# Optimization experiments

Measured on AMD Instinct MI355X. Metric: run time of the kernel, lower is better.

## Reference

```python
import jax, jax.numpy as jnp
import numpy as np

WH = WW = 7          # window size
N_TOK = WH * WW      # 49 tokens per window
HEADS = 8
HEAD_DIM = 32
DIM = HEADS * HEAD_DIM  # 256
NW = 64              # windows per image (56x56 / 7x7)
BW = 64 * NW         # batch_images * windows = 4096


def _rel_pos_index(wh, ww):
    # Swin-style relative position index, flattened to (N*N,)
    coords = np.stack(np.meshgrid(np.arange(wh), np.arange(ww), indexing='ij'))  # (2, wh, ww)
    coords = coords.reshape(2, -1)                                               # (2, N)
    rel = coords[:, :, None] - coords[:, None, :]                                # (2, N, N)
    rel = rel.transpose(1, 2, 0).astype(np.int64)                                # (N, N, 2)
    rel[:, :, 0] += wh - 1
    rel[:, :, 1] += ww - 1
    rel[:, :, 0] *= 2 * ww - 1
    return jnp.asarray(rel.sum(-1).reshape(-1))                                  # (N*N,)

_REL_IDX = _rel_pos_index(WH, WW)


def setup_inputs() -> dict:
    key = jax.random.key(0)
    ks = jax.random.split(key, 5)
    x = jax.random.normal(ks[0], (BW, N_TOK, DIM), dtype=jnp.float32)
    mask = jnp.zeros((1, NW, 1, N_TOK, N_TOK), dtype=jnp.float32)
    w_qkv = jax.random.normal(ks[1], (DIM, 3 * HEADS * HEAD_DIM), dtype=jnp.float32) * 0.02
    b_qkv = jnp.zeros((3 * HEADS * HEAD_DIM,), dtype=jnp.float32)
    rel_table = jax.random.normal(ks[2], ((2 * WH - 1) * (2 * WW - 1), HEADS), dtype=jnp.float32) * 0.02
    w_out = jax.random.normal(ks[3], (HEADS * HEAD_DIM, DIM), dtype=jnp.float32) * 0.02
    b_out = jnp.zeros((DIM,), dtype=jnp.float32)
    return {"x": x, "mask": mask, "w_qkv": w_qkv, "b_qkv": b_qkv,
            "rel_table": rel_table, "w_out": w_out, "b_out": b_out}


def reference(x, mask, w_qkv, b_qkv, rel_table, w_out, b_out):
    bw, n, d = x.shape
    # QKV projection then split per original Rearrange:
    # 'b n (qkv h hd) -> qkv b h n hd'
    qkv = (x @ w_qkv + b_qkv).reshape(bw, n, 3, HEADS, HEAD_DIM)
    qkv = qkv.transpose(2, 0, 3, 1, 4)  # (3, bw, h, n, hd)
    q, k, v = qkv[0], qkv[1], qkv[2]
    # NOTE: original computes einsum('bnid,bnjd->bnij', k, q): a[i,j] = k_i . q_j
    a = jnp.einsum('bhid,bhjd->bhij', k, q) / jnp.sqrt(jnp.asarray(HEAD_DIM, x.dtype))
    # relative position bias: table gather then '(i j) h -> h i j'
    bias = rel_table[_REL_IDX].reshape(n, n, HEADS).transpose(2, 0, 1)  # (h, n, n)
    a = a + bias
    # mask add: '(b nW) h i j -> b nW h i j', + mask, back
    nw = mask.shape[1]
    a = a.reshape(bw // nw, nw, HEADS, n, n) + mask
    a = a.reshape(bw, HEADS, n, n)
    a = jax.nn.softmax(a, axis=-1)
    y = jnp.einsum('bhij,bhjd->bhid', a, v)        # (bw, h, n, hd)
    y = y.transpose(0, 2, 1, 3).reshape(bw, n, HEADS * HEAD_DIM)
    return y @ w_out + b_out
```

## Files before the change

kernel.cpp:

```cpp
#include <hip/hip_runtime.h>

typedef __attribute__((ext_vector_type(8))) short short8;
typedef __attribute__((ext_vector_type(4))) float f32x4;
typedef unsigned short u16;

#define NTOK 49
#define NBLK 4096
#define LOG2E 1.4426950408889634f

#define XF  0
#define QKP 16384
#define VTF 49152
#define POOLN 65536

#define WS_WQT 0
#define WS_WOT 393216
#define WS_BQS 524288
#define WS_BIAS 528384
#define WS_MKG 659456
#define WS_CMB 1708032
#define WS_NEED (WS_CMB + 8388608)

__device__ __forceinline__ u16 f2bf(float f) {
  unsigned u = __float_as_uint(f);
  return (u16)((u + 0x7fffu + ((u >> 16) & 1u)) >> 16);
}
__device__ __forceinline__ unsigned packbf(float a, float b) {
  unsigned r;
  asm("v_cvt_pk_bf16_f32 %0, %1, %2" : "=v"(r) : "v"(a), "v"(b));
  return r;
}

__global__ void prep_kernel(const float* __restrict__ w_qkv,
                            const float* __restrict__ w_out,
                            const float* __restrict__ rel,
                            const float* __restrict__ mask,
                            const float* __restrict__ b_qkv,
                            u16* __restrict__ wqTf,
                            u16* __restrict__ woTf,
                            float* __restrict__ bqs,
                            float* __restrict__ biasf,
                            float* __restrict__ mkg) {
  const float SCQ = 0.17677669529663687f * LOG2E;
  const int stride = gridDim.x * blockDim.x;
  const int gid = blockIdx.x * blockDim.x + threadIdx.x;
  for (int e = gid; e < 48 * 8 * 64 * 8; e += stride) {
    int eL = e & 7, ln = (e >> 3) & 63, ks = (e >> 9) & 7, ctg = e >> 12;
    int k = ks * 32 + (ln >> 4) * 8 + eL;
    int c = ctg * 16 + (ln & 15);
    float wv = w_qkv[k * 768 + c];
    if (ctg < 16) wv *= SCQ;
    wqTf[e] = f2bf(wv);
  }
  for (int e = gid; e < 16 * 8 * 64 * 8; e += stride) {
    int eL = e & 7, ln = (e >> 3) & 63, ks = (e >> 9) & 7, ctg = e >> 12;
    int k = ks * 32 + (ln >> 4) * 8 + eL;
    int c = ctg * 16 + (ln & 15);
    woTf[e] = f2bf(w_out[k * 256 + c]);
  }
  for (int e = gid; e < 768; e += stride)
    bqs[e] = b_qkv[e] * (e < 256 ? SCQ : 1.f);
  for (int e = gid; e < 8 * 16 * 64 * 4; e += stride) {
    int rg = e & 3, ln = (e >> 2) & 63, t = (e >> 8) & 15, hh = e >> 12;
    int i = (t >> 2) * 16 + (ln & 15);
    int j = (t & 3) * 16 + (ln >> 4) * 4 + rg;
    float v;
    if (j >= NTOK) v = -1e30f;
    else if (i >= NTOK) v = 0.f;
    else {
      int dh = i / 7 - j / 7 + 6;
      int dw = i % 7 - j % 7 + 6;
      v = rel[(dh * 13 + dw) * 8 + hh];
    }
    biasf[e] = v * LOG2E;
  }
  for (int e = gid; e < 64 * 16 * 64 * 4; e += stride) {
    int rg = e & 3, ln = (e >> 2) & 63, t = (e >> 8) & 15, wdw = e >> 12;
    int i = (t >> 2) * 16 + (ln & 15);
    int j = (t & 3) * 16 + (ln >> 4) * 4 + rg;
    mkg[e] = (i < NTOK && j < NTOK) ? mask[wdw * (NTOK * NTOK) + i * NTOK + j] * LOG2E : 0.f;
  }
}

__global__ void prep2_kernel(const float* __restrict__ biasf,
                             const float* __restrict__ mkg,
                             float* __restrict__ cmb) {
  const int stride = gridDim.x * blockDim.x;
  for (int e = blockIdx.x * blockDim.x + threadIdx.x; e < 64 * 8 * 4096; e += stride) {
    int x = e & 4095, hh = (e >> 12) & 7, wdw = e >> 15;
    cmb[e] = biasf[hh * 4096 + x] + mkg[wdw * 4096 + x];
  }
}

__global__ void __launch_bounds__(1024, 4) winattn_mfma(
    const float* __restrict__ x,
    const float* __restrict__ bqs,
    const float* __restrict__ b_out,
    const u16* __restrict__ wqTf,
    const u16* __restrict__ woTf,
    const float* __restrict__ biasf,
    const float* __restrict__ mkg,
    const float* __restrict__ cmb,
    float* __restrict__ out)
{
  __shared__ u16 pool[POOLN];
  const int b = blockIdx.x, tid = threadIdx.x;
  const int lane = tid & 63, lo = lane & 15, hi = lane >> 4;
  const int w = tid >> 6;
  const int h = w & 7;
  const int it0 = (w >> 3) * 2;
  const f32x4 zf = {0.f, 0.f, 0.f, 0.f};

  {
    const float4* xg = (const float4*)(x + (size_t)b * (NTOK * 256));
    for (int e = tid; e < 49 * 64; e += 1024) {
      float4 v = xg[e];
      int r = e >> 6, c4 = (e & 63) << 2;
      int addr = (((r >> 4) * 8 + (c4 >> 5)) * 64 + ((c4 >> 3) & 3) * 16 + (r & 15)) * 8 + (c4 & 7);
      *(uint2*)&pool[XF + addr] = make_uint2(packbf(v.x, v.y), packbf(v.z, v.w));
    }
    if (tid < 15 * 64) {
      int e = tid;
      int r = 49 + (e >> 6), c4 = (e & 63) << 2;
      int addr = (((r >> 4) * 8 + (c4 >> 5)) * 64 + ((c4 >> 3) & 3) * 16 + (r & 15)) * 8 + (c4 & 7);
      *(uint2*)&pool[XF + addr] = make_uint2(0u, 0u);
    }
  }
  __syncthreads();

  {
    const int ctq0 = 2 * w, ctq1 = 2 * w + 1, ctv = 32 + w;
    f32x4 acc[3][4];
    #pragma unroll
    for (int ct = 0; ct < 3; ++ct)
      #pragma unroll
      for (int rt = 0; rt < 4; ++rt) acc[ct][rt] = zf;
    #pragma unroll
    for (int ks = 0; ks < 8; ++ks) {
      short8 bx[4];
      #pragma unroll
      for (int rt = 0; rt < 4; ++rt)
        bx[rt] = *(const short8*)&pool[XF + ((rt * 8 + ks) * 64 + lane) * 8];
      short8 af0 = *(const short8*)&wqTf[((size_t)(ctq0 * 8 + ks) * 64 + lane) * 8];
      short8 af1 = *(const short8*)&wqTf[((size_t)(ctq1 * 8 + ks) * 64 + lane) * 8];
      short8 afv = *(const short8*)&wqTf[((size_t)(ctv * 8 + ks) * 64 + lane) * 8];
      #pragma unroll
      for (int rt = 0; rt < 4; ++rt) {
        acc[0][rt] = __builtin_amdgcn_mfma_f32_16x16x32_bf16(af0, bx[rt], acc[0][rt], 0, 0, 0);
        acc[1][rt] = __builtin_amdgcn_mfma_f32_16x16x32_bf16(af1, bx[rt], acc[1][rt], 0, 0, 0);
        acc[2][rt] = __builtin_amdgcn_mfma_f32_16x16x32_bf16(bx[rt], afv, acc[2][rt], 0, 0, 0);
      }
    }
    const int qkbase = QKP + (w & 7) * 4096 + ((w >= 8) ? 2048 : 0);
    #pragma unroll
    for (int ct = 0; ct < 2; ++ct) {
      const int ctg = 2 * w + ct;
      f32x4 bias = *(const f32x4*)(bqs + ctg * 16 + hi * 4);
      #pragma unroll
      for (int rt = 0; rt < 4; ++rt) {
        f32x4 v = acc[ct][rt] + bias;
        int hi2 = ct * 2 + (hi >> 1);
        int eb = (hi & 1) * 4;
        *(uint2*)&pool[qkbase + (rt * 64 + hi2 * 16 + lo) * 8 + eb] =
            make_uint2(packbf(v[0], v[1]), packbf(v[2], v[3]));
      }
    }
    {
      const int vhead = w >> 1, dblk = w & 1;
      const float bv = bqs[ctv * 16 + lo];
      #pragma unroll
      for (int rt = 0; rt < 4; ++rt) {
        f32x4 v = acc[2][rt];
        float v0 = v[0] + bv, v1 = v[1] + bv, v2 = v[2] + bv, v3 = v[3] + bv;
        int f = dblk * 2 + (rt >> 1);
        int hiR = (rt & 1) * 2 + (hi >> 1);
        int eb = (hi & 1) * 4;
        *(uint2*)&pool[VTF + (f * 8 + vhead) * 512 + (hiR * 16 + lo) * 8 + eb] =
            make_uint2(packbf(v0, v1), packbf(v2, v3));
      }
    }
  }
  __syncthreads();

  short8 va[2][2];
  #pragma unroll
  for (int dblk = 0; dblk < 2; ++dblk)
    #pragma unroll
    for (int k2 = 0; k2 < 2; ++k2)
      va[dblk][k2] = *(const short8*)&pool[VTF + ((dblk * 2 + k2) * 8 + h) * 512 + lane * 8];
  __syncthreads();

  {
    short8 qa[4], ka[2];
    #pragma unroll
    for (int jt = 0; jt < 4; ++jt)
      qa[jt] = *(const short8*)&pool[QKP + h * 4096 + (jt * 64 + lane) * 8];
    #pragma unroll
    for (int itL = 0; itL < 2; ++itL)
      ka[itL] = *(const short8*)&pool[QKP + h * 4096 + 2048 + ((it0 + itL) * 64 + lane) * 8];
    const float* cb;
    const float* mb = nullptr;
    if (cmb) {
      cb = cmb + (((size_t)(b & 63) * 8 + h) << 12);
    } else {
      cb = biasf + h * 4096;
      mb = mkg + (size_t)(b & 63) * 4096;
    }
    #pragma unroll
    for (int itL = 0; itL < 2; ++itL) {
      float rs = 0.f;
      #pragma unroll
      for (int jt = 0; jt < 4; ++jt) {
        f32x4 s = __builtin_amdgcn_mfma_f32_16x16x32_bf16(qa[jt], ka[itL], zf, 0, 0, 0);
        const int t = (it0 + itL) * 4 + jt;
        f32x4 c4 = *(const f32x4*)&cb[(t * 64 + lane) * 4];
        if (mb) {
          f32x4 m4 = *(const f32x4*)&mb[(t * 64 + lane) * 4];
          c4[0] += m4[0]; c4[1] += m4[1]; c4[2] += m4[2]; c4[3] += m4[3];
        }
        float p0 = exp2f(s[0] + c4[0]);
        float p1 = exp2f(s[1] + c4[1]);
        float p2 = exp2f(s[2] + c4[2]);
        float p3 = exp2f(s[3] + c4[3]);
        rs += (p0 + p1) + (p2 + p3);
        int k2 = jt >> 1;
        int hi2 = (jt & 1) * 2 + (hi >> 1);
        int eb = (hi & 1) * 4;
        *(uint2*)&pool[VTF + ((it0 + k2) * 8 + h) * 512 + (hi2 * 16 + lo) * 8 + eb] =
            make_uint2(packbf(p0, p1), packbf(p2, p3));
      }
      float r2 = rs + __shfl_xor(rs, 16);
      const float inv = 1.f / (r2 + __shfl_xor(r2, 32));
      f32x4 ya0 = zf, ya1 = zf;
      #pragma unroll
      for (int k2 = 0; k2 < 2; ++k2) {
        short8 pb = *(const short8*)&pool[VTF + ((it0 + k2) * 8 + h) * 512 + lane * 8];
        ya0 = __builtin_amdgcn_mfma_f32_16x16x32_bf16(va[0][k2], pb, ya0, 0, 0, 0);
        ya1 = __builtin_amdgcn_mfma_f32_16x16x32_bf16(va[1][k2], pb, ya1, 0, 0, 0);
      }
      #pragma unroll
      for (int dblk = 0; dblk < 2; ++dblk) {
        f32x4 yy = dblk ? ya1 : ya0;
        int hi2 = dblk * 2 + (hi >> 1);
        int eb = (hi & 1) * 4;
        *(uint2*)&pool[XF + (((it0 + itL) * 8 + h) * 64 + hi2 * 16 + lo) * 8 + eb] =
            make_uint2(packbf(yy[0] * inv, yy[1] * inv), packbf(yy[2] * inv, yy[3] * inv));
      }
    }
  }
  __syncthreads();

  {
    f32x4 pacc[4];
    pacc[0] = zf; pacc[1] = zf; pacc[2] = zf; pacc[3] = zf;
    #pragma unroll
    for (int ks = 0; ks < 8; ++ks) {
      short8 wf = *(const short8*)&woTf[((size_t)(w * 8 + ks) * 64 + lane) * 8];
      #pragma unroll
      for (int rt = 0; rt < 4; ++rt) {
        short8 yb = *(const short8*)&pool[XF + ((rt * 8 + ks) * 64 + lane) * 8];
        pacc[rt] = __builtin_amdgcn_mfma_f32_16x16x32_bf16(wf, yb, pacc[rt], 0, 0, 0);
      }
    }
    float* og = out + (size_t)b * (NTOK * 256);
    const int cb2 = w * 16 + hi * 4;
    f32x4 bb = *(const f32x4*)(b_out + cb2);
    #pragma unroll
    for (int rt = 0; rt < 4; ++rt) {
      const int r = rt * 16 + lo;
      if (r < NTOK) {
        f32x4 vv = pacc[rt] + bb;
        *(f32x4*)(og + (size_t)r * 256 + cb2) = vv;
      }
    }
  }
}

extern "C" void kernel_launch(void* const* d_in, const int* in_sizes, int n_in,
                              void* d_out, int out_size, void* d_ws, size_t ws_size,
                              hipStream_t stream) {
  const float *x = nullptr, *mask = nullptr, *w_qkv = nullptr, *b_qkv = nullptr,
              *rel_t = nullptr, *w_out = nullptr, *b_out = nullptr;
  for (int i = 0; i < n_in; ++i) {
    const float* p = (const float*)d_in[i];
    switch (in_sizes[i]) {
      case 4096 * 49 * 256: x = p; break;
      case 64 * 49 * 49:    mask = p; break;
      case 256 * 768:       w_qkv = p; break;
      case 768:             b_qkv = p; break;
      case 169 * 8:         rel_t = p; break;
      case 256 * 256:       w_out = p; break;
      case 256:             b_out = p; break;
    }
  }
  char* wsb = (char*)d_ws;
  u16* wqTf    = (u16*)(wsb + WS_WQT);
  u16* woTf    = (u16*)(wsb + WS_WOT);
  float* bqs   = (float*)(wsb + WS_BQS);
  float* biasf = (float*)(wsb + WS_BIAS);
  float* mkg   = (float*)(wsb + WS_MKG);
  const bool fits = (ws_size >= (size_t)WS_NEED);
  float* cmb   = fits ? (float*)(wsb + WS_CMB) : nullptr;

  hipLaunchKernelGGL(prep_kernel, dim3(1024), dim3(256), 0, stream,
                     w_qkv, w_out, rel_t, mask, b_qkv, wqTf, woTf, bqs, biasf, mkg);
  if (fits) {
    hipLaunchKernelGGL(prep2_kernel, dim3(2048), dim3(256), 0, stream,
                       biasf, mkg, cmb);
  }
  hipLaunchKernelGGL(winattn_mfma, dim3(NBLK), dim3(1024), 0, stream,
                     x, bqs, b_out, wqTf, woTf, biasf, mkg, cmb, (float*)d_out);
}
```

Measured before the change: 279.1 us.

## Process two windows per block and prefetch second window's input during attention

Each 1024-thread block now handles two consecutive windows instead of one, halving the grid. The second window's x tile is loaded and converted to bf16 into a free region of shared memory while the first window's softmax and PV stage runs, so global load latency can overlap with compute. The shared-memory layout is remapped so the second window's QK buffers avoid the staged x region. The cost is extra barriers and fewer blocks in flight, which gives the scheduler less parallelism to hide latency across the GPU.

```diff
diff --git a/kernel.cpp b/kernel.cpp
--- a/kernel.cpp
+++ b/kernel.cpp
@@ -5,11 +5,8 @@
 typedef unsigned short u16;
 
 #define NTOK 49
-#define NBLK 4096
 #define LOG2E 1.4426950408889634f
 
-#define XF  0
-#define QKP 16384
 #define VTF 49152
 #define POOLN 65536
 
@@ -92,6 +89,22 @@
   }
 }
 
+__device__ __forceinline__ void stage_x(const float4* __restrict__ xg,
+                                        u16* __restrict__ pool, int base, int tid) {
+  for (int e = tid; e < 49 * 64; e += 1024) {
+    float4 v = xg[e];
+    int r = e >> 6, c4 = (e & 63) << 2;
+    int addr = (((r >> 4) * 8 + (c4 >> 5)) * 64 + ((c4 >> 3) & 3) * 16 + (r & 15)) * 8 + (c4 & 7);
+    *(uint2*)&pool[base + addr] = make_uint2(packbf(v.x, v.y), packbf(v.z, v.w));
+  }
+  if (tid < 15 * 64) {
+    int e = tid;
+    int r = 49 + (e >> 6), c4 = (e & 63) << 2;
+    int addr = (((r >> 4) * 8 + (c4 >> 5)) * 64 + ((c4 >> 3) & 3) * 16 + (r & 15)) * 8 + (c4 & 7);
+    *(uint2*)&pool[base + addr] = make_uint2(0u, 0u);
+  }
+}
+
 __global__ void __launch_bounds__(1024, 4) winattn_mfma(
     const float* __restrict__ x,
     const float* __restrict__ bqs,
@@ -104,175 +117,179 @@
     float* __restrict__ out)
 {
   __shared__ u16 pool[POOLN];
-  const int b = blockIdx.x, tid = threadIdx.x;
+  const int tid = threadIdx.x;
   const int lane = tid & 63, lo = lane & 15, hi = lane >> 4;
   const int w = tid >> 6;
   const int h = w & 7;
   const int it0 = (w >> 3) * 2;
   const f32x4 zf = {0.f, 0.f, 0.f, 0.f};
-
-  {
-    const float4* xg = (const float4*)(x + (size_t)b * (NTOK * 256));
-    for (int e = tid; e < 49 * 64; e += 1024) {
-      float4 v = xg[e];
-      int r = e >> 6, c4 = (e & 63) << 2;
-      int addr = (((r >> 4) * 8 + (c4 >> 5)) * 64 + ((c4 >> 3) & 3) * 16 + (r & 15)) * 8 + (c4 & 7);
-      *(uint2*)&pool[XF + addr] = make_uint2(packbf(v.x, v.y), packbf(v.z, v.w));
-    }
-    if (tid < 15 * 64) {
-      int e = tid;
-      int r = 49 + (e >> 6), c4 = (e & 63) << 2;
-      int addr = (((r >> 4) * 8 + (c4 >> 5)) * 64 + ((c4 >> 3) & 3) * 16 + (r & 15)) * 8 + (c4 & 7);
-      *(uint2*)&pool[XF + addr] = make_uint2(0u, 0u);
-    }
-  }
+  const int b0 = blockIdx.x * 2;
+
+  stage_x((const float4*)(x + (size_t)b0 * (NTOK * 256)), pool, 0, tid);
   __syncthreads();
 
-  {
-    const int ctq0 = 2 * w, ctq1 = 2 * w + 1, ctv = 32 + w;
-    f32x4 acc[3][4];
+  #pragma unroll
+  for (int wi = 0; wi < 2; ++wi) {
+    const int b2 = b0 + wi;
+    const int xb = wi ? 16384 : 0;
+    const int qkhb = wi ? ((h < 4) ? h * 4096 : 32768 + (h - 4) * 4096)
+                        : 16384 + h * 4096;
+
+    {
+      const int ctq0 = 2 * w, ctq1 = 2 * w + 1, ctv = 32 + w;
+      f32x4 acc[3][4];
+      #pragma unroll
+      for (int ct = 0; ct < 3; ++ct)
+        #pragma unroll
+        for (int rt = 0; rt < 4; ++rt) acc[ct][rt] = zf;
+      #pragma unroll
+      for (int ks = 0; ks < 8; ++ks) {
+        short8 bx[4];
+        #pragma unroll
+        for (int rt = 0; rt < 4; ++rt)
+          bx[rt] = *(const short8*)&pool[xb + ((rt * 8 + ks) * 64 + lane) * 8];
+        short8 af0 = *(const short8*)&wqTf[((size_t)(ctq0 * 8 + ks) * 64 + lane) * 8];
+        short8 af1 = *(const short8*)&wqTf[((size_t)(ctq1 * 8 + ks) * 64 + lane) * 8];
+        short8 afv = *(const short8*)&wqTf[((size_t)(ctv * 8 + ks) * 64 + lane) * 8];
+        #pragma unroll
+        for (int rt = 0; rt < 4; ++rt) {
+          acc[0][rt] = __builtin_amdgcn_mfma_f32_16x16x32_bf16(af0, bx[rt], acc[0][rt], 0, 0, 0);
+          acc[1][rt] = __builtin_amdgcn_mfma_f32_16x16x32_bf16(af1, bx[rt], acc[1][rt], 0, 0, 0);
+          acc[2][rt] = __builtin_amdgcn_mfma_f32_16x16x32_bf16(bx[rt], afv, acc[2][rt], 0, 0, 0);
+        }
+      }
+      const int qkw = wi ? (((w & 7) < 4) ? (w & 7) * 4096 : 32768 + ((w & 7) - 4) * 4096)
+                         : 16384 + (w & 7) * 4096;
+      const int qkbase = qkw + ((w >= 8) ? 2048 : 0);
+      #pragma unroll
+      for (int ct = 0; ct < 2; ++ct) {
+        const int ctg = 2 * w + ct;
+        f32x4 bias = *(const f32x4*)(bqs + ctg * 16 + hi * 4);
+        #pragma unroll
+        for (int rt = 0; rt < 4; ++rt) {
+          f32x4 v = acc[ct][rt] + bias;
+          int hi2 = ct * 2 + (hi >> 1);
+          int eb = (hi & 1) * 4;
+          *(uint2*)&pool[qkbase + (rt * 64 + hi2 * 16 + lo) * 8 + eb] =
+              make_uint2(packbf(v[0], v[1]), packbf(v[2], v[3]));
+        }
+      }
+      {
+        const int vhead = w >> 1, dblk = w & 1;
+        const float bv = bqs[ctv * 16 + lo];
+        #pragma unroll
+        for (int rt = 0; rt < 4; ++rt) {
+          f32x4 v = acc[2][rt];
+          float v0 = v[0] + bv, v1 = v[1] + bv, v2 = v[2] + bv, v3 = v[3] + bv;
+          int f = dblk * 2 + (rt >> 1);
+          int hiR = (rt & 1) * 2 + (hi >> 1);
+          int eb = (hi & 1) * 4;
+          *(uint2*)&pool[VTF + (f * 8 + vhead) * 512 + (hiR * 16 + lo) * 8 + eb] =
+              make_uint2(packbf(v0, v1), packbf(v2, v3));
+        }
+      }
+    }
+    __syncthreads();
+
+    short8 va[2][2];
     #pragma unroll
-    for (int ct = 0; ct < 3; ++ct)
-      #pragma unroll
-      for (int rt = 0; rt < 4; ++rt) acc[ct][rt] = zf;
-    #pragma unroll
-    for (int ks = 0; ks < 8; ++ks) {
-      short8 bx[4];
-      #pragma unroll
-      for (int rt = 0; rt < 4; ++rt)
-        bx[rt] = *(const short8*)&pool[XF + ((rt * 8 + ks) * 64 + lane) * 8];
-      short8 af0 = *(const short8*)&wqTf[((size_t)(ctq0 * 8 + ks) * 64 + lane) * 8];
-      short8 af1 = *(const short8*)&wqTf[((size_t)(ctq1 * 8 + ks) * 64 + lane) * 8];
-      short8 afv = *(const short8*)&wqTf[((size_t)(ctv * 8 + ks) * 64 + lane) * 8];
-      #pragma unroll
-      for (int rt = 0; rt < 4; ++rt) {
-        acc[0][rt] = __builtin_amdgcn_mfma_f32_16x16x32_bf16(af0, bx[rt], acc[0][rt], 0, 0, 0);
-        acc[1][rt] = __builtin_amdgcn_mfma_f32_16x16x32_bf16(af1, bx[rt], acc[1][rt], 0, 0, 0);
-        acc[2][rt] = __builtin_amdgcn_mfma_f32_16x16x32_bf16(bx[rt], afv, acc[2][rt], 0, 0, 0);
-      }
-    }
-    const int qkbase = QKP + (w & 7) * 4096 + ((w >= 8) ? 2048 : 0);
-    #pragma unroll
-    for (int ct = 0; ct < 2; ++ct) {
-      const int ctg = 2 * w + ct;
-      f32x4 bias = *(const f32x4*)(bqs + ctg * 16 + hi * 4);
-      #pragma unroll
-      for (int rt = 0; rt < 4; ++rt) {
-        f32x4 v = acc[ct][rt] + bias;
-        int hi2 = ct * 2 + (hi >> 1);
-        int eb = (hi & 1) * 4;
-        *(uint2*)&pool[qkbase + (rt * 64 + hi2 * 16 + lo) * 8 + eb] =
-            make_uint2(packbf(v[0], v[1]), packbf(v[2], v[3]));
-      }
-    }
-    {
-      const int vhead = w >> 1, dblk = w & 1;
-      const float bv = bqs[ctv * 16 + lo];
-      #pragma unroll
-      for (int rt = 0; rt < 4; ++rt) {
-        f32x4 v = acc[2][rt];
-        float v0 = v[0] + bv, v1 = v[1] + bv, v2 = v[2] + bv, v3 = v[3] + bv;
-        int f = dblk * 2 + (rt >> 1);
-        int hiR = (rt & 1) * 2 + (hi >> 1);
-        int eb = (hi & 1) * 4;
-        *(uint2*)&pool[VTF + (f * 8 + vhead) * 512 + (hiR * 16 + lo) * 8 + eb] =
-            make_uint2(packbf(v0, v1), packbf(v2, v3));
-      }
-    }
-  }
-  __syncthreads();
-
-  short8 va[2][2];
-  #pragma unroll
-  for (int dblk = 0; dblk < 2; ++dblk)
-    #pragma unroll
-    for (int k2 = 0; k2 < 2; ++k2)
-      va[dblk][k2] = *(const short8*)&pool[VTF + ((dblk * 2 + k2) * 8 + h) * 512 + lane * 8];
-  __syncthreads();
-
-  {
+    for (int dblk = 0; dblk < 2; ++dblk)
+      #pragma unroll
+      for (int k2 = 0; k2 < 2; ++k2)
+        va[dblk][k2] = *(const short8*)&pool[VTF + ((dblk * 2 + k2) * 8 + h) * 512 + lane * 8];
+    __syncthreads();
+
     short8 qa[4], ka[2];
     #pragma unroll
     for (int jt = 0; jt < 4; ++jt)
-      qa[jt] = *(const short8*)&pool[QKP + h * 4096 + (jt * 64 + lane) * 8];
+      qa[jt] = *(const short8*)&pool[qkhb + (jt * 64 + lane) * 8];
     #pragma unroll
     for (int itL = 0; itL < 2; ++itL)
-      ka[itL] = *(const short8*)&pool[QKP + h * 4096 + 2048 + ((it0 + itL) * 64 + lane) * 8];
-    const float* cb;
-    const float* mb = nullptr;
-    if (cmb) {
-      cb = cmb + (((size_t)(b & 63) * 8 + h) << 12);
-    } else {
-      cb = biasf + h * 4096;
-      mb = mkg + (size_t)(b & 63) * 4096;
-    }
-    #pragma unroll
-    for (int itL = 0; itL < 2; ++itL) {
-      float rs = 0.f;
-      #pragma unroll
-      for (int jt = 0; jt < 4; ++jt) {
-        f32x4 s = __builtin_amdgcn_mfma_f32_16x16x32_bf16(qa[jt], ka[itL], zf, 0, 0, 0);
-        const int t = (it0 + itL) * 4 + jt;
-        f32x4 c4 = *(const f32x4*)&cb[(t * 64 + lane) * 4];
-        if (mb) {
-          f32x4 m4 = *(const f32x4*)&mb[(t * 64 + lane) * 4];
-          c4[0] += m4[0]; c4[1] += m4[1]; c4[2] += m4[2]; c4[3] += m4[3];
-        }
-        float p0 = exp2f(s[0] + c4[0]);
-        float p1 = exp2f(s[1] + c4[1]);
-        float p2 = exp2f(s[2] + c4[2]);
-        float p3 = exp2f(s[3] + c4[3]);
-        rs += (p0 + p1) + (p2 + p3);
-        int k2 = jt >> 1;
-        int hi2 = (jt & 1) * 2 + (hi >> 1);
-        int eb = (hi & 1) * 4;
-        *(uint2*)&pool[VTF + ((it0 + k2) * 8 + h) * 512 + (hi2 * 16 + lo) * 8 + eb] =
-            make_uint2(packbf(p0, p1), packbf(p2, p3));
-      }
-      float r2 = rs + __shfl_xor(rs, 16);
-      const float inv = 1.f / (r2 + __shfl_xor(r2, 32));
-      f32x4 ya0 = zf, ya1 = zf;
-      #pragma unroll
-      for (int k2 = 0; k2 < 2; ++k2) {
-        short8 pb = *(const short8*)&pool[VTF + ((it0 + k2) * 8 + h) * 512 + lane * 8];
-        ya0 = __builtin_amdgcn_mfma_f32_16x16x32_bf16(va[0][k2], pb, ya0, 0, 0, 0);
-        ya1 = __builtin_amdgcn_mfma_f32_16x16x32_bf16(va[1][k2], pb, ya1, 0, 0, 0);
-      }
-      #pragma unroll
-      for (int dblk = 0; dblk < 2; ++dblk) {
-        f32x4 yy = dblk ? ya1 : ya0;
-        int hi2 = dblk * 2 + (hi >> 1);
-        int eb = (hi & 1) * 4;
-        *(uint2*)&pool[XF + (((it0 + itL) * 8 + h) * 64 + hi2 * 16 + lo) * 8 + eb] =
-            make_uint2(packbf(yy[0] * inv, yy[1] * inv), packbf(yy[2] * inv, yy[3] * inv));
-      }
-    }
-  }
-  __syncthreads();
-
-  {
-    f32x4 pacc[4];
-    pacc[0] = zf; pacc[1] = zf; pacc[2] = zf; pacc[3] = zf;
-    #pragma unroll
-    for (int ks = 0; ks < 8; ++ks) {
-      short8 wf = *(const short8*)&woTf[((size_t)(w * 8 + ks) * 64 + lane) * 8];
+      ka[itL] = *(const short8*)&pool[qkhb + 2048 + ((it0 + itL) * 64 + lane) * 8];
+
+    if (wi == 0) {
+      __syncthreads();
+      stage_x((const float4*)(x + (size_t)(b0 + 1) * (NTOK * 256)), pool, 16384, tid);
+    }
+
+    {
+      const float* cb;
+      const float* mb = nullptr;
+      if (cmb) {
+        cb = cmb + (((size_t)(b2 & 63) * 8 + h) << 12);
+      } else {
+        cb = biasf + h * 4096;
+        mb = mkg + (size_t)(b2 & 63) * 4096;
+      }
+      #pragma unroll
+      for (int itL = 0; itL < 2; ++itL) {
+        float rs = 0.f;
+        #pragma unroll
+        for (int jt = 0; jt < 4; ++jt) {
+          f32x4 s = __builtin_amdgcn_mfma_f32_16x16x32_bf16(qa[jt], ka[itL], zf, 0, 0, 0);
+          const int t = (it0 + itL) * 4 + jt;
+          f32x4 c4 = *(const f32x4*)&cb[(t * 64 + lane) * 4];
+          if (mb) {
+            f32x4 m4 = *(const f32x4*)&mb[(t * 64 + lane) * 4];
+            c4[0] += m4[0]; c4[1] += m4[1]; c4[2] += m4[2]; c4[3] += m4[3];
+          }
+          float p0 = exp2f(s[0] + c4[0]);
+          float p1 = exp2f(s[1] + c4[1]);
+          float p2 = exp2f(s[2] + c4[2]);
+          float p3 = exp2f(s[3] + c4[3]);
+          rs += (p0 + p1) + (p2 + p3);
+          int k2 = jt >> 1;
+          int hi2 = (jt & 1) * 2 + (hi >> 1);
+          int eb = (hi & 1) * 4;
+          *(uint2*)&pool[VTF + ((it0 + k2) * 8 + h) * 512 + (hi2 * 16 + lo) * 8 + eb] =
+              make_uint2(packbf(p0, p1), packbf(p2, p3));
+        }
+        float r2 = rs + __shfl_xor(rs, 16);
+        const float inv = 1.f / (r2 + __shfl_xor(r2, 32));
+        f32x4 ya0 = zf, ya1 = zf;
+        #pragma unroll
+        for (int k2 = 0; k2 < 2; ++k2) {
+          short8 pb = *(const short8*)&pool[VTF + ((it0 + k2) * 8 + h) * 512 + lane * 8];
+          ya0 = __builtin_amdgcn_mfma_f32_16x16x32_bf16(va[0][k2], pb, ya0, 0, 0, 0);
+          ya1 = __builtin_amdgcn_mfma_f32_16x16x32_bf16(va[1][k2], pb, ya1, 0, 0, 0);
+        }
+        #pragma unroll
+        for (int dblk = 0; dblk < 2; ++dblk) {
+          f32x4 yy = dblk ? ya1 : ya0;
+          int hi2 = dblk * 2 + (hi >> 1);
+          int eb = (hi & 1) * 4;
+          *(uint2*)&pool[xb + (((it0 + itL) * 8 + h) * 64 + hi2 * 16 + lo) * 8 + eb] =
+              make_uint2(packbf(yy[0] * inv, yy[1] * inv), packbf(yy[2] * inv, yy[3] * inv));
+        }
+      }
+    }
+    __syncthreads();
+
+    {
+      f32x4 pacc[4];
+      pacc[0] = zf; pacc[1] = zf; pacc[2] = zf; pacc[3] = zf;
+      #pragma unroll
+      for (int ks = 0; ks < 8; ++ks) {
+        short8 wf = *(const short8*)&woTf[((size_t)(w * 8 + ks) * 64 + lane) * 8];
+        #pragma unroll
+        for (int rt = 0; rt < 4; ++rt) {
+          short8 yb = *(const short8*)&pool[xb + ((rt * 8 + ks) * 64 + lane) * 8];
+          pacc[rt] = __builtin_amdgcn_mfma_f32_16x16x32_bf16(wf, yb, pacc[rt], 0, 0, 0);
+        }
+      }
+      float* og = out + (size_t)b2 * (NTOK * 256);
+      const int cb2 = w * 16 + hi * 4;
+      f32x4 bb = *(const f32x4*)(b_out + cb2);
       #pragma unroll
       for (int rt = 0; rt < 4; ++rt) {
-        short8 yb = *(const short8*)&pool[XF + ((rt * 8 + ks) * 64 + lane) * 8];
-        pacc[rt] = __builtin_amdgcn_mfma_f32_16x16x32_bf16(wf, yb, pacc[rt], 0, 0, 0);
-      }
-    }
-    float* og = out + (size_t)b * (NTOK * 256);
-    const int cb2 = w * 16 + hi * 4;
-    f32x4 bb = *(const f32x4*)(b_out + cb2);
-    #pragma unroll
-    for (int rt = 0; rt < 4; ++rt) {
-      const int r = rt * 16 + lo;
-      if (r < NTOK) {
-        f32x4 vv = pacc[rt] + bb;
-        *(f32x4*)(og + (size_t)r * 256 + cb2) = vv;
-      }
-    }
+        const int r = rt * 16 + lo;
+        if (r < NTOK) {
+          f32x4 vv = pacc[rt] + bb;
+          *(f32x4*)(og + (size_t)r * 256 + cb2) = vv;
+        }
+      }
+    }
+    if (wi == 0) __syncthreads();
   }
 }
 
@@ -308,6 +325,6 @@
     hipLaunchKernelGGL(prep2_kernel, dim3(2048), dim3(256), 0, stream,
                        biasf, mkg, cmb);
   }
-  hipLaunchKernelGGL(winattn_mfma, dim3(NBLK), dim3(1024), 0, stream,
+  hipLaunchKernelGGL(winattn_mfma, dim3(2048), dim3(1024), 0, stream,
                      x, bqs, b_out, wqTf, woTf, biasf, mkg, cmb, (float*)d_out);
 }
```

After: 364.7 us. 30.7% more time.
